# Kernel optimization log

Measured on AMD Instinct MI355X. Metric: run time of the kernel, lower is better.

The kernel has to match this reference:

```python
import jax, jax.numpy as jnp
import numpy as np

DIM = 1024
HEADS = 16
SEQ = 1024
N_EXP = 2
SLOTS = SEQ // N_EXP  # slots per expert; total slots == seq_len as in SoftMoE(dim, seq_len, num_experts)
HID = 4 * DIM         # expert FFN hidden
EPS = 1e-5


def layernorm(x, g, b):
    mu = x.mean(-1, keepdims=True)
    var = x.var(-1, keepdims=True)
    return (x - mu) * jax.lax.rsqrt(var + EPS) * g + b


def setup_inputs() -> dict:
    key = jax.random.key(0)
    ks = jax.random.split(key, 16)
    s = lambda k, shape, scale=0.02: jax.random.normal(k, shape, jnp.float32) * scale
    return {
        "x": jax.random.normal(ks[0], (4, SEQ, DIM), jnp.float32),
        "Wq": s(ks[1], (DIM, DIM)), "bq": jnp.zeros((DIM,), jnp.float32),
        "Wkv": s(ks[2], (DIM, 2 * DIM)), "bkv": jnp.zeros((2 * DIM,), jnp.float32),
        "Wp": s(ks[3], (DIM, DIM)), "bp": jnp.zeros((DIM,), jnp.float32),
        "g1": jnp.ones((DIM,), jnp.float32), "b1": jnp.zeros((DIM,), jnp.float32),
        "phi": s(ks[4], (DIM, N_EXP, SLOTS)),
        "We1": s(ks[5], (N_EXP, DIM, HID)), "be1": jnp.zeros((N_EXP, HID), jnp.float32),
        "We2": s(ks[6], (N_EXP, HID, DIM)), "be2": jnp.zeros((N_EXP, DIM), jnp.float32),
        "g2": jnp.ones((DIM,), jnp.float32), "b2": jnp.zeros((DIM,), jnp.float32),
    }


def soft_moe(x, phi, We1, be1, We2, be2):
    # x: [b,n,d]; phi: [d,e,s]
    logits = jnp.einsum("bnd,des->bnes", x, phi)
    dispatch = jax.nn.softmax(logits, axis=1)                    # over sequence
    b, n, e, s = logits.shape
    combine = jax.nn.softmax(logits.reshape(b, n, e * s), axis=-1).reshape(b, n, e, s)
    slots = jnp.einsum("bnd,bnes->besd", x, dispatch)            # [b,e,s,d]
    h = jax.nn.gelu(jnp.einsum("besd,edh->besh", slots, We1) + be1[None, :, None, :])
    y = jnp.einsum("besh,ehd->besd", h, We2) + be2[None, :, None, :]
    return jnp.einsum("besd,bnes->bnd", y, combine)


def reference(x, Wq, bq, Wkv, bkv, Wp, bp, g1, b1, phi, We1, be1, We2, be2, g2, b2):
    b, n, c = x.shape
    hd = c // HEADS
    scale = hd ** -0.5
    q = (x @ Wq + bq).reshape(b, n, HEADS, hd)
    kv = (x @ Wkv + bkv).reshape(b, n, 2, HEADS, hd)
    k, v = kv[:, :, 0], kv[:, :, 1]
    attn = jnp.einsum("bnhd,bmhd->bnmh", q, k) * scale
    attn = jax.nn.softmax(attn, axis=2)
    out = jnp.einsum("bnmh,bmhd->bnhd", attn, v).reshape(b, n, c)
    out = out @ Wp + bp
    x1 = layernorm(out + x, g1, b1)
    x2 = x1 + soft_moe(x1, phi, We1, be1, We2, be2)
    y = layernorm(x2 + x1, g2, b2)
    return (y, attn)
```

## Files before the change

kernel.cpp:

```cpp
#include <hip/hip_runtime.h>
#include <math.h>

#define BATCH 4
#define SEQ   1024
#define DIM   1024
#define HEADS 16
#define HD    64
#define NEXP  2
#define NSLOT 512
#define ES    1024
#define HID   4096
#define LNEPS 1e-5f
#define NTOK  (BATCH*SEQ)

typedef long long ll;
typedef unsigned short ushort;
typedef unsigned int uint;
typedef __attribute__((ext_vector_type(8))) short short8;
typedef __attribute__((ext_vector_type(4))) float f32x4;
typedef __attribute__((ext_vector_type(4))) unsigned short us4;

__device__ __forceinline__ ushort f2b(float f) {
    uint u = __builtin_bit_cast(uint, f);
    u += 0x7FFFu + ((u >> 16) & 1u);
    return (ushort)(u >> 16);
}
__device__ __forceinline__ float b2f(ushort h) {
    uint u = ((uint)h) << 16;
    return __builtin_bit_cast(float, u);
}
__device__ __forceinline__ uint pk(float a, float b) {
    return (uint)f2b(a) | ((uint)f2b(b) << 16);
}
__device__ __forceinline__ float gelu_f(float v) {
    float x3 = v * v * v;
    return 0.5f * v * (1.f + tanhf(0.7978845608028654f * (v + 0.044715f * x3)));
}

__device__ __forceinline__ void gload16(const ushort* g, ushort* l) {
    __builtin_amdgcn_global_load_lds(
        (const __attribute__((address_space(1))) unsigned int*)(const void*)g,
        (__attribute__((address_space(3))) unsigned int*)(void*)l,
        16, 0, 0);
}

__global__ __launch_bounds__(256) void cvt_bf16(
    const float* __restrict__ src, ushort* __restrict__ dst)
{
    int i = blockIdx.x * 256 + threadIdx.x;
    const float4* s = reinterpret_cast<const float4*>(src) + (ll)i * 2;
    float4 a = s[0], b = s[1];
    uint4 w;
    w.x = pk(a.x, a.y); w.y = pk(a.z, a.w);
    w.z = pk(b.x, b.y); w.w = pk(b.z, b.w);
    reinterpret_cast<uint4*>(dst)[i] = w;
}

__global__ __launch_bounds__(256) void concat_bias(
    const float* __restrict__ a, const float* __restrict__ b,
    float* __restrict__ o)
{
    int i = blockIdx.x * 256 + threadIdx.x;
    o[i] = (i < DIM) ? a[i] : b[i - DIM];
}

template<typename TS, typename TD>
__global__ __launch_bounds__(256) void transpose_cvt(
    const TS* __restrict__ src, int ldsrc, ll sS1, ll sS2,
    TD* __restrict__ dst, int lddst, ll sD1, ll sD2, int Z2)
{
    __shared__ TD tile[64][68];
    const int z1 = blockIdx.z / Z2, z2 = blockIdx.z % Z2;
    src += z1 * sS1 + z2 * sS2;
    dst += z1 * sD1 + z2 * sD2;
    const int r0 = blockIdx.y * 64, c0 = blockIdx.x * 64;
    const int t = threadIdx.x;
    #pragma unroll
    for (int j = 0; j < 4; j++) {
        int idx = t + 256 * j;
        int r = idx >> 4, c = (idx & 15) * 4;
        if constexpr (sizeof(TS) == 4 && sizeof(TD) == 2) {
            float4 v = *reinterpret_cast<const float4*>(src + (ll)(r0 + r) * ldsrc + c0 + c);
            tile[r][c]     = f2b(v.x);
            tile[r][c + 1] = f2b(v.y);
            tile[r][c + 2] = f2b(v.z);
            tile[r][c + 3] = f2b(v.w);
        } else if constexpr (sizeof(TS) == 4 && sizeof(TD) == 4) {
            float4 v = *reinterpret_cast<const float4*>(src + (ll)(r0 + r) * ldsrc + c0 + c);
            *reinterpret_cast<float4*>(&tile[r][c]) = v;
        } else {
            *reinterpret_cast<us4*>(&tile[r][c]) =
                *reinterpret_cast<const us4*>(src + (ll)(r0 + r) * ldsrc + c0 + c);
        }
    }
    __syncthreads();
    #pragma unroll
    for (int j = 0; j < 4; j++) {
        int idx = t + 256 * j;
        int rr = idx >> 4, cc = (idx & 15) * 4;
        if constexpr (sizeof(TD) == 2) {
            us4 w;
            w.x = tile[cc][rr]; w.y = tile[cc + 1][rr];
            w.z = tile[cc + 2][rr]; w.w = tile[cc + 3][rr];
            *reinterpret_cast<us4*>(&dst[(ll)(c0 + rr) * lddst + r0 + cc]) = w;
        } else {
            float4 w;
            w.x = tile[cc][rr]; w.y = tile[cc + 1][rr];
            w.z = tile[cc + 2][rr]; w.w = tile[cc + 3][rr];
            *reinterpret_cast<float4*>(&dst[(ll)(c0 + rr) * lddst + r0 + cc]) = w;
        }
    }
}

template<int WR, int WC, int MI, int NI, int ACT, typename TC>
__global__ __launch_bounds__(256) void gemm_bf16(
    const ushort* __restrict__ A, int lda, ll sA1, ll sA2,
    const ushort* __restrict__ B, int ldb, ll sB1, ll sB2,
    const float* __restrict__ bias, ll sb1, ll sb2,
    TC* __restrict__ C, int ldc, ll sC1, ll sC2,
    int K, int Z2, float alpha)
{
    constexpr int BM = WR * MI * 16;
    constexpr int BN = WC * NI * 16;
    __shared__ alignas(16) ushort As[BM * 32];
    __shared__ alignas(16) ushort Bs[BN * 32];

    const int z1 = blockIdx.z / Z2, z2 = blockIdx.z % Z2;
    A += z1 * sA1 + z2 * sA2;
    B += z1 * sB1 + z2 * sB2;
    C += z1 * sC1 + z2 * sC2;

    const int t = threadIdx.x;
    const int m0 = blockIdx.y * BM, n0 = blockIdx.x * BN;
    const int lane = t & 63, wave = t >> 6;
    const int quad = lane >> 4, l16 = lane & 15;
    const int wm = wave / WC, wn = wave % WC;

    f32x4 acc[MI][NI] = {};

    for (int k0 = 0; k0 < K; k0 += 32) {
        #pragma unroll
        for (int i = 0; i < BM / 64; i++) {
            int seg = i * 256 + t;
            int row = seg >> 2, ke = (seg & 3) * 8;
            gload16(A + (ll)(m0 + row) * lda + (k0 + ke), &As[seg * 8]);
        }
        #pragma unroll
        for (int i = 0; i < BN / 64; i++) {
            int seg = i * 256 + t;
            int row = seg >> 2, ke = (seg & 3) * 8;
            gload16(B + (ll)(n0 + row) * ldb + (k0 + ke), &Bs[seg * 8]);
        }
        __syncthreads();

        short8 a[MI], b[NI];
        #pragma unroll
        for (int mi = 0; mi < MI; mi++)
            a[mi] = *reinterpret_cast<const short8*>(
                &As[(wm * MI * 16 + mi * 16 + l16) * 32 + quad * 8]);
        #pragma unroll
        for (int ni = 0; ni < NI; ni++)
            b[ni] = *reinterpret_cast<const short8*>(
                &Bs[(wn * NI * 16 + ni * 16 + l16) * 32 + quad * 8]);
        #pragma unroll
        for (int mi = 0; mi < MI; mi++)
            #pragma unroll
            for (int ni = 0; ni < NI; ni++)
                acc[mi][ni] = __builtin_amdgcn_mfma_f32_16x16x32_bf16(
                    a[mi], b[ni], acc[mi][ni], 0, 0, 0);
        __syncthreads();
    }

    const float* bz = bias ? (bias + z1 * sb1 + z2 * sb2) : nullptr;
    #pragma unroll
    for (int mi = 0; mi < MI; mi++) {
        #pragma unroll
        for (int ni = 0; ni < NI; ni++) {
            const int row = m0 + wm * MI * 16 + mi * 16 + quad * 4;
            const int col = n0 + wn * NI * 16 + ni * 16 + l16;
            const float bv = bz ? bz[col] : 0.f;
            #pragma unroll
            for (int r = 0; r < 4; r++) {
                float v = alpha * acc[mi][ni][r] + bv;
                if (ACT) v = gelu_f(v);
                if constexpr (sizeof(TC) == 2)
                    C[(ll)(row + r) * ldc + col] = f2b(v);
                else
                    C[(ll)(row + r) * ldc + col] = v;
            }
        }
    }
}

template<int BM, int BN, int ACT, typename TC>
__global__ __launch_bounds__(512) void gemm2(
    const ushort* __restrict__ A, int lda, ll sA1, ll sA2,
    const ushort* __restrict__ B, int ldb, ll sB1, ll sB2,
    const float* __restrict__ bias, ll sb1, ll sb2,
    TC* __restrict__ C, int ldc, ll sC1, ll sC2,
    int K, int Z2, float alpha)
{
    constexpr int WR = BM / 64;
    constexpr int WC = 8 / WR;
    constexpr int MI = 4;
    constexpr int NI = BN / WC / 16;
    constexpr int NH = NI / 2 ? NI / 2 : 1;
    constexpr int LA = BM / 64;
    constexpr int LB = BN / 64;

    __shared__ alignas(16) ushort As[3][BM * 64];
    __shared__ alignas(16) ushort Bs[3][BN * 64];

    const int z1 = blockIdx.z / Z2, z2 = blockIdx.z % Z2;
    A += z1 * sA1 + z2 * sA2;
    B += z1 * sB1 + z2 * sB2;
    C += z1 * sC1 + z2 * sC2;

    const int t = threadIdx.x;
    const int lane = t & 63, wave = t >> 6;
    const int quad = lane >> 4, l16 = lane & 15;
    const int wm = wave / WC, wn = wave % WC;
    const int m0 = blockIdx.y * BM, n0 = blockIdx.x * BN;

    auto stageA = [&](int kt) {
        const ushort* src = A + (ll)m0 * lda + kt * 64;
        ushort* dst = As[kt % 3];
        #pragma unroll
        for (int j = 0; j < LA; j++) {
            int seg = j * 512 + t;
            int row = seg >> 3, kk = (seg & 7) * 8;
            gload16(src + (ll)row * lda + kk, dst + seg * 8);
        }
    };
    auto stageB = [&](int kt) {
        const ushort* src = B + (ll)n0 * ldb + kt * 64;
        ushort* dst = Bs[kt % 3];
        #pragma unroll
        for (int j = 0; j < LB; j++) {
            int seg = j * 512 + t;
            int row = seg >> 3, kk = (seg & 7) * 8;
            gload16(src + (ll)row * ldb + kk, dst + seg * 8);
        }
    };

    f32x4 acc[MI][NI] = {};
    const int NK = K / 64;

    stageA(0); stageB(0);
    if (NK > 1) { stageA(1); stageB(1); }

    for (int kt = 0; kt < NK; kt++) {
        if (kt + 1 < NK)
            asm volatile("s_waitcnt vmcnt(%0)" :: "n"(LA + LB) : "memory");
        else
            asm volatile("s_waitcnt vmcnt(0)" ::: "memory");
        __builtin_amdgcn_sched_barrier(0);
        __builtin_amdgcn_s_barrier();
        __builtin_amdgcn_sched_barrier(0);

        const ushort* Abuf = As[kt % 3];
        const ushort* Bbuf = Bs[kt % 3];

        short8 a[MI][2], b0[NH][2];
        #pragma unroll
        for (int mi = 0; mi < MI; mi++)
            #pragma unroll
            for (int kh = 0; kh < 2; kh++)
                a[mi][kh] = *reinterpret_cast<const short8*>(
                    &Abuf[(wm * 64 + mi * 16 + l16) * 64 + kh * 32 + quad * 8]);
        #pragma unroll
        for (int ni = 0; ni < NH; ni++)
            #pragma unroll
            for (int kh = 0; kh < 2; kh++)
                b0[ni][kh] = *reinterpret_cast<const short8*>(
                    &Bbuf[(wn * NI * 16 + ni * 16 + l16) * 64 + kh * 32 + quad * 8]);
        if (kt + 2 < NK) stageA(kt + 2);
        asm volatile("s_waitcnt lgkmcnt(0)" ::: "memory");
        __builtin_amdgcn_sched_barrier(0);
        __builtin_amdgcn_s_setprio(1);
        #pragma unroll
        for (int mi = 0; mi < MI; mi++)
            #pragma unroll
            for (int ni = 0; ni < NH; ni++)
                #pragma unroll
                for (int kh = 0; kh < 2; kh++)
                    acc[mi][ni] = __builtin_amdgcn_mfma_f32_16x16x32_bf16(
                        a[mi][kh], b0[ni][kh], acc[mi][ni], 0, 0, 0);
        __builtin_amdgcn_s_setprio(0);
        __builtin_amdgcn_sched_barrier(0);

        short8 b1[NH][2];
        #pragma unroll
        for (int ni = 0; ni < NH; ni++)
            #pragma unroll
            for (int kh = 0; kh < 2; kh++)
                b1[ni][kh] = *reinterpret_cast<const short8*>(
                    &Bbuf[(wn * NI * 16 + (NH + ni) * 16 + l16) * 64 + kh * 32 + quad * 8]);
        if (kt + 2 < NK) stageB(kt + 2);
        asm volatile("s_waitcnt lgkmcnt(0)" ::: "memory");
        __builtin_amdgcn_sched_barrier(0);
        __builtin_amdgcn_s_setprio(1);
        #pragma unroll
        for (int mi = 0; mi < MI; mi++)
            #pragma unroll
            for (int ni = 0; ni < NH; ni++)
                #pragma unroll
                for (int kh = 0; kh < 2; kh++)
                    acc[mi][NH + ni] = __builtin_amdgcn_mfma_f32_16x16x32_bf16(
                        a[mi][kh], b1[ni][kh], acc[mi][NH + ni], 0, 0, 0);
        __builtin_amdgcn_s_setprio(0);
        __builtin_amdgcn_sched_barrier(0);
    }

    const float* bz = bias ? (bias + z1 * sb1 + z2 * sb2) : nullptr;
    #pragma unroll
    for (int mi = 0; mi < MI; mi++) {
        #pragma unroll
        for (int ni = 0; ni < NI; ni++) {
            const int row = m0 + wm * 64 + mi * 16 + quad * 4;
            const int col = n0 + wn * NI * 16 + ni * 16 + l16;
            const float bv = bz ? bz[col] : 0.f;
            #pragma unroll
            for (int r = 0; r < 4; r++) {
                float v = alpha * acc[mi][ni][r] + bv;
                if (ACT) v = gelu_f(v);
                if constexpr (sizeof(TC) == 2)
                    C[(ll)(row + r) * ldc + col] = f2b(v);
                else
                    C[(ll)(row + r) * ldc + col] = v;
            }
        }
    }
}

__global__ __launch_bounds__(256) void attn_softmax(
    ushort* __restrict__ p, float* __restrict__ attn_out)
{
    __shared__ float tile[16][1024];
    const int n = blockIdx.x, b = blockIdx.y;
    const int t = threadIdx.x;
    const int lane = t & 63, w = t >> 6;
    ushort* base = p + ((ll)(b * SEQ + n) * HEADS) * SEQ;
    #pragma unroll 1
    for (int g = 0; g < 4; g++) {
        const int h = g * 4 + w;
        ushort* row = base + (ll)h * SEQ + lane * 16;
        uint4 r0 = reinterpret_cast<const uint4*>(row)[0];
        uint4 r1 = reinterpret_cast<const uint4*>(row)[1];
        uint rr[8] = {r0.x, r0.y, r0.z, r0.w, r1.x, r1.y, r1.z, r1.w};
        float v[16];
        float m = -3.0e38f;
        #pragma unroll
        for (int j = 0; j < 8; j++) {
            v[2 * j]     = b2f((ushort)(rr[j] & 0xFFFFu));
            v[2 * j + 1] = b2f((ushort)(rr[j] >> 16));
            m = fmaxf(m, fmaxf(v[2 * j], v[2 * j + 1]));
        }
        #pragma unroll
        for (int o = 32; o; o >>= 1) m = fmaxf(m, __shfl_xor(m, o));
        float s = 0.f;
        #pragma unroll
        for (int j = 0; j < 16; j++) { v[j] = __expf(v[j] - m); s += v[j]; }
        #pragma unroll
        for (int o = 32; o; o >>= 1) s += __shfl_xor(s, o);
        const float inv = 1.f / s;
        #pragma unroll
        for (int j = 0; j < 16; j++) v[j] *= inv;
        uint pw[8];
        #pragma unroll
        for (int j = 0; j < 8; j++) pw[j] = pk(v[2 * j], v[2 * j + 1]);
        uint4 w0, w1;
        w0.x = pw[0]; w0.y = pw[1]; w0.z = pw[2]; w0.w = pw[3];
        w1.x = pw[4]; w1.y = pw[5]; w1.z = pw[6]; w1.w = pw[7];
        reinterpret_cast<uint4*>(row)[0] = w0;
        reinterpret_cast<uint4*>(row)[1] = w1;
        #pragma unroll
        for (int jj = 0; jj < 4; jj++) {
            float4 f4;
            f4.x = v[4 * jj]; f4.y = v[4 * jj + 1];
            f4.z = v[4 * jj + 2]; f4.w = v[4 * jj + 3];
            *reinterpret_cast<float4*>(&tile[h][(jj * 64 + lane) * 4]) = f4;
        }
    }
    __syncthreads();
    float* outp = attn_out + ((ll)b * SEQ + n) * SEQ * HEADS;
    #pragma unroll
    for (int jj = 0; jj < 4; jj++) {
        const int mm = t + 256 * jj;
        const int gm = mm >> 2;
        const int fi = ((gm & 3) * 64 + (gm >> 2)) * 4 + (mm & 3);
        float o16[16];
        #pragma unroll
        for (int h = 0; h < 16; h++) o16[h] = tile[h][fi];
        float4* dst = reinterpret_cast<float4*>(outp + (ll)mm * HEADS);
        #pragma unroll
        for (int q = 0; q < 4; q++) {
            float4 o4;
            o4.x = o16[4 * q]; o4.y = o16[4 * q + 1];
            o4.z = o16[4 * q + 2]; o4.w = o16[4 * q + 3];
            dst[q] = o4;
        }
    }
}

__global__ __launch_bounds__(256) void ln_kernel(
    const float* __restrict__ a, const float* __restrict__ b, float coef,
    const float* __restrict__ g, const float* __restrict__ beta,
    float* __restrict__ out, ushort* __restrict__ out_bf)
{
    const int row = blockIdx.x;
    const int t = threadIdx.x;
    float4 av = reinterpret_cast<const float4*>(a + (ll)row * DIM)[t];
    float4 bv = reinterpret_cast<const float4*>(b + (ll)row * DIM)[t];
    float4 v;
    v.x = av.x + coef * bv.x; v.y = av.y + coef * bv.y;
    v.z = av.z + coef * bv.z; v.w = av.w + coef * bv.w;
    float s1 = v.x + v.y + v.z + v.w;
    float s2 = v.x * v.x + v.y * v.y + v.z * v.z + v.w * v.w;
    __shared__ float red[8];
    #pragma unroll
    for (int o = 32; o; o >>= 1) { s1 += __shfl_xor(s1, o); s2 += __shfl_xor(s2, o); }
    int w = t >> 6;
    if ((t & 63) == 0) { red[w] = s1; red[4 + w] = s2; }
    __syncthreads();
    s1 = red[0] + red[1] + red[2] + red[3];
    s2 = red[4] + red[5] + red[6] + red[7];
    float mu = s1 * (1.f / DIM);
    float var = s2 * (1.f / DIM) - mu * mu;
    float rs = rsqrtf(var + LNEPS);
    float4 gv = reinterpret_cast<const float4*>(g)[t];
    float4 be = reinterpret_cast<const float4*>(beta)[t];
    float4 o;
    o.x = (v.x - mu) * rs * gv.x + be.x;
    o.y = (v.y - mu) * rs * gv.y + be.y;
    o.z = (v.z - mu) * rs * gv.z + be.z;
    o.w = (v.w - mu) * rs * gv.w + be.w;
    reinterpret_cast<float4*>(out + (ll)row * DIM)[t] = o;
    if (out_bf) {
        us4 hv;
        hv.x = f2b(o.x); hv.y = f2b(o.y); hv.z = f2b(o.z); hv.w = f2b(o.w);
        reinterpret_cast<us4*>(out_bf + (ll)row * DIM)[t] = hv;
    }
}

__global__ __launch_bounds__(256) void row_softmax(
    const float* __restrict__ logits, ushort* __restrict__ comb)
{
    const int row = blockIdx.x;
    const int t = threadIdx.x;
    float4 v = reinterpret_cast<const float4*>(logits + (ll)row * 1024)[t];
    float m = fmaxf(fmaxf(v.x, v.y), fmaxf(v.z, v.w));
    __shared__ float red[8];
    #pragma unroll
    for (int o = 32; o; o >>= 1) m = fmaxf(m, __shfl_xor(m, o));
    int w = t >> 6;
    if ((t & 63) == 0) red[w] = m;
    __syncthreads();
    m = fmaxf(fmaxf(red[0], red[1]), fmaxf(red[2], red[3]));
    __syncthreads();
    float4 e;
    e.x = __expf(v.x - m); e.y = __expf(v.y - m);
    e.z = __expf(v.z - m); e.w = __expf(v.w - m);
    float s = e.x + e.y + e.z + e.w;
    #pragma unroll
    for (int o = 32; o; o >>= 1) s += __shfl_xor(s, o);
    if ((t & 63) == 0) red[4 + w] = s;
    __syncthreads();
    s = red[4] + red[5] + red[6] + red[7];
    float inv = 1.f / s;
    us4 hv;
    hv.x = f2b(e.x * inv); hv.y = f2b(e.y * inv);
    hv.z = f2b(e.z * inv); hv.w = f2b(e.w * inv);
    reinterpret_cast<us4*>(comb + (ll)row * 1024)[t] = hv;
}

extern "C" void kernel_launch(void* const* d_in, const int* in_sizes, int n_in,
                              void* d_out, int out_size, void* d_ws, size_t ws_size,
                              hipStream_t stream)
{
    const float* x   = (const float*)d_in[0];
    const float* Wq  = (const float*)d_in[1];
    const float* bq  = (const float*)d_in[2];
    const float* Wkv = (const float*)d_in[3];
    const float* bkv = (const float*)d_in[4];
    const float* Wp  = (const float*)d_in[5];
    const float* bp  = (const float*)d_in[6];
    const float* g1  = (const float*)d_in[7];
    const float* b1  = (const float*)d_in[8];
    const float* phi = (const float*)d_in[9];
    const float* We1 = (const float*)d_in[10];
    const float* be1 = (const float*)d_in[11];
    const float* We2 = (const float*)d_in[12];
    const float* be2 = (const float*)d_in[13];
    const float* g2  = (const float*)d_in[14];
    const float* b2  = (const float*)d_in[15];

    float* out_y    = (float*)d_out;
    float* out_attn = out_y + (ll)BATCH * SEQ * DIM;

    const ll M1 = 1024 * 1024;
    float*  ws     = (float*)d_ws;
    ushort* x_bf   = (ushort*)(ws);
    ushort* WqkvT  = (ushort*)(ws + 2 * M1);
    ushort* WpT    = (ushort*)(ws + 7 * M1 / 2);
    ushort* phiT   = (ushort*)(ws + 4 * M1);
    ushort* qkv_bf = (ushort*)(ws + 9 * M1 / 2);
    ushort* vT     = (ushort*)(ws + 21 * M1 / 2);
    ushort* p_bf   = (ushort*)(ws + 25 * M1 / 2);
    float*  po     = ws + 25 * M1 / 2;
    float*  logitT = ws + 25 * M1 / 2;
    ushort* ao_bf  = (ushort*)(ws + 89 * M1 / 2);
    ushort* ymoeT  = (ushort*)(ws + 89 * M1 / 2);
    float*  x1     = ws + 33 * M1 / 2;
    ushort* x1_bf  = (ushort*)(ws + 41 * M1 / 2);
    ushort* x1T    = (ushort*)(ws + 45 * M1 / 2);
    float*  logit  = ws + 49 * M1 / 2;
    ushort* dispT  = (ushort*)(ws + 57 * M1 / 2);
    ushort* comb   = (ushort*)(ws + 61 * M1 / 2);
    ushort* slots  = (ushort*)(ws + 65 * M1 / 2);
    ushort* hmid   = (ushort*)(ws + 69 * M1 / 2);
    ushort* ymoe   = (ushort*)(ws + 85 * M1 / 2);
    ushort* We1T   = (ushort*)(ws + 9 * M1 / 2);
    ushort* We2T   = (ushort*)(ws + 17 * M1 / 2);
    float*  bqkv   = ws + 93 * M1 / 2;
    float*  moe    = ws;

    dim3 blk(256), blk5(512);

    cvt_bf16<<<dim3(2048), blk, 0, stream>>>(x, x_bf);
    transpose_cvt<float,ushort><<<dim3(16, 16, 1), blk, 0, stream>>>(
        Wq, DIM, 0, 0, WqkvT, DIM, 0, 0, 1);
    transpose_cvt<float,ushort><<<dim3(32, 16, 1), blk, 0, stream>>>(
        Wkv, 2 * DIM, 0, 0, WqkvT + (ll)DIM * DIM, DIM, 0, 0, 1);
    transpose_cvt<float,ushort><<<dim3(16, 16, 1), blk, 0, stream>>>(
        Wp, DIM, 0, 0, WpT, DIM, 0, 0, 1);
    transpose_cvt<float,ushort><<<dim3(16, 16, 1), blk, 0, stream>>>(
        phi, ES, 0, 0, phiT, DIM, 0, 0, 1);
    concat_bias<<<dim3(12), blk, 0, stream>>>(bq, bkv, bqkv);

    gemm2<256,128,0,ushort><<<dim3(24, 16, 1), blk5, 0, stream>>>(
        x_bf, DIM, 0, 0, WqkvT, DIM, 0, 0, bqkv, 0, 0,
        qkv_bf, 3 * DIM, 0, 0, DIM, 1, 1.f);

    transpose_cvt<ushort,ushort><<<dim3(1, 16, BATCH * HEADS), blk, 0, stream>>>(
        qkv_bf + 2 * DIM, 3 * DIM, (ll)SEQ * 3 * DIM, HD,
        vT, SEQ, (ll)HEADS * HD * SEQ, (ll)HD * SEQ, HEADS);

    gemm_bf16<2,2,4,4,0,ushort><<<dim3(8, 8, BATCH * HEADS), blk, 0, stream>>>(
        qkv_bf, 3 * DIM, (ll)SEQ * 3 * DIM, HD,
        qkv_bf + DIM, 3 * DIM, (ll)SEQ * 3 * DIM, HD,
        nullptr, 0, 0,
        p_bf, HEADS * SEQ, (ll)SEQ * HEADS * SEQ, (ll)SEQ,
        HD, HEADS, 0.125f);

    attn_softmax<<<dim3(SEQ, BATCH), blk, 0, stream>>>(p_bf, out_attn);

    gemm2<256,64,0,ushort><<<dim3(1, 4, BATCH * HEADS), blk5, 0, stream>>>(
        p_bf, HEADS * SEQ, (ll)SEQ * HEADS * SEQ, (ll)SEQ,
        vT, SEQ, (ll)HEADS * HD * SEQ, (ll)HD * SEQ,
        nullptr, 0, 0,
        ao_bf, DIM, (ll)SEQ * DIM, HD,
        SEQ, HEADS, 1.f);

    gemm2<128,128,0,float><<<dim3(8, 32, 1), blk5, 0, stream>>>(
        ao_bf, DIM, 0, 0, WpT, DIM, 0, 0, bp, 0, 0,
        po, DIM, 0, 0, DIM, 1, 1.f);
    ln_kernel<<<dim3(NTOK), blk, 0, stream>>>(po, x, 1.0f, g1, b1, x1, x1_bf);

    transpose_cvt<float,ushort><<<dim3(64, 16, 2), blk, 0, stream>>>(
        We1, HID, 0, (ll)DIM * HID, We1T, DIM, 0, (ll)HID * DIM, 2);
    transpose_cvt<float,ushort><<<dim3(16, 64, 2), blk, 0, stream>>>(
        We2, DIM, 0, (ll)HID * DIM, We2T, HID, 0, (ll)DIM * HID, 2);
    transpose_cvt<ushort,ushort><<<dim3(16, 16, BATCH), blk, 0, stream>>>(
        x1_bf, DIM, (ll)SEQ * DIM, 0, x1T, SEQ, (ll)DIM * SEQ, 0, 1);

    gemm2<128,128,0,float><<<dim3(8, 32, 1), blk5, 0, stream>>>(
        x1_bf, DIM, 0, 0, phiT, DIM, 0, 0, nullptr, 0, 0,
        logit, ES, 0, 0, DIM, 1, 1.f);

    transpose_cvt<float,float><<<dim3(16, 16, BATCH), blk, 0, stream>>>(
        logit, ES, (ll)SEQ * ES, 0, logitT, SEQ, (ll)ES * SEQ, 0, 1);
    row_softmax<<<dim3(BATCH * ES), blk, 0, stream>>>(logitT, dispT);
    row_softmax<<<dim3(NTOK), blk, 0, stream>>>(logit, comb);

    gemm2<128,128,0,ushort><<<dim3(8, 8, BATCH), blk5, 0, stream>>>(
        dispT, SEQ, (ll)ES * SEQ, 0,
        x1T, SEQ, (ll)DIM * SEQ, 0,
        nullptr, 0, 0,
        slots, DIM, (ll)ES * DIM, 0,
        SEQ, 1, 1.f);

    gemm2<256,128,1,ushort><<<dim3(32, 2, BATCH * NEXP), blk5, 0, stream>>>(
        slots, DIM, (ll)ES * DIM, (ll)NSLOT * DIM,
        We1T, DIM, 0, (ll)HID * DIM,
        be1, 0, HID,
        hmid, HID, (ll)ES * HID, (ll)NSLOT * HID,
        DIM, NEXP, 1.f);

    gemm2<128,128,0,ushort><<<dim3(8, 4, BATCH * NEXP), blk5, 0, stream>>>(
        hmid, HID, (ll)ES * HID, (ll)NSLOT * HID,
        We2T, HID, 0, (ll)DIM * HID,
        be2, 0, DIM,
        ymoe, DIM, (ll)ES * DIM, (ll)NSLOT * DIM,
        HID, NEXP, 1.f);

    transpose_cvt<ushort,ushort><<<dim3(16, 16, BATCH), blk, 0, stream>>>(
        ymoe, DIM, (ll)ES * DIM, 0, ymoeT, ES, (ll)DIM * ES, 0, 1);

    gemm2<128,128,0,float><<<dim3(8, 8, BATCH), blk5, 0, stream>>>(
        comb, ES, (ll)SEQ * ES, 0,
        ymoeT, ES, (ll)DIM * ES, 0,
        nullptr, 0, 0,
        moe, DIM, (ll)SEQ * DIM, 0,
        ES, 1, 1.f);

    ln_kernel<<<dim3(NTOK), blk, 0, stream>>>(moe, x1, 2.0f, g2, b2, out_y, nullptr);
}
```

Measured before the change: 883.6 us.

## Replace 512-thread triple-buffered GEMMs with 256-thread double-buffered gemm2d kernel

After: 940.7 us. 1.06x slower.

```diff
diff --git a/kernel.cpp b/kernel.cpp
--- a/kernel.cpp
+++ b/kernel.cpp
@@ -112,18 +112,21 @@
     }
 }
 
-template<int WR, int WC, int MI, int NI, int ACT, typename TC>
-__global__ __launch_bounds__(256) void gemm_bf16(
+template<int BM, int BN, int NBUF, int ACT, typename TC>
+__global__ __launch_bounds__(256) void gemm2d(
     const ushort* __restrict__ A, int lda, ll sA1, ll sA2,
     const ushort* __restrict__ B, int ldb, ll sB1, ll sB2,
     const float* __restrict__ bias, ll sb1, ll sb2,
     TC* __restrict__ C, int ldc, ll sC1, ll sC2,
     int K, int Z2, float alpha)
 {
-    constexpr int BM = WR * MI * 16;
-    constexpr int BN = WC * NI * 16;
-    __shared__ alignas(16) ushort As[BM * 32];
-    __shared__ alignas(16) ushort Bs[BN * 32];
+    constexpr int MI = BM / 32;
+    constexpr int NI = BN / 32;
+    constexpr int LA = BM / 32;
+    constexpr int LB = BN / 32;
+
+    __shared__ alignas(16) ushort As[NBUF][BM * 64];
+    __shared__ alignas(16) ushort Bs[NBUF][BN * 64];
 
     const int z1 = blockIdx.z / Z2, z2 = blockIdx.z % Z2;
     A += z1 * sA1 + z2 * sA2;
@@ -131,113 +134,27 @@
     C += z1 * sC1 + z2 * sC2;
 
     const int t = threadIdx.x;
-    const int m0 = blockIdx.y * BM, n0 = blockIdx.x * BN;
     const int lane = t & 63, wave = t >> 6;
     const int quad = lane >> 4, l16 = lane & 15;
-    const int wm = wave / WC, wn = wave % WC;
-
-    f32x4 acc[MI][NI] = {};
-
-    for (int k0 = 0; k0 < K; k0 += 32) {
-        #pragma unroll
-        for (int i = 0; i < BM / 64; i++) {
-            int seg = i * 256 + t;
-            int row = seg >> 2, ke = (seg & 3) * 8;
-            gload16(A + (ll)(m0 + row) * lda + (k0 + ke), &As[seg * 8]);
-        }
-        #pragma unroll
-        for (int i = 0; i < BN / 64; i++) {
-            int seg = i * 256 + t;
-            int row = seg >> 2, ke = (seg & 3) * 8;
-            gload16(B + (ll)(n0 + row) * ldb + (k0 + ke), &Bs[seg * 8]);
-        }
-        __syncthreads();
-
-        short8 a[MI], b[NI];
-        #pragma unroll
-        for (int mi = 0; mi < MI; mi++)
-            a[mi] = *reinterpret_cast<const short8*>(
-                &As[(wm * MI * 16 + mi * 16 + l16) * 32 + quad * 8]);
-        #pragma unroll
-        for (int ni = 0; ni < NI; ni++)
-            b[ni] = *reinterpret_cast<const short8*>(
-                &Bs[(wn * NI * 16 + ni * 16 + l16) * 32 + quad * 8]);
-        #pragma unroll
-        for (int mi = 0; mi < MI; mi++)
-            #pragma unroll
-            for (int ni = 0; ni < NI; ni++)
-                acc[mi][ni] = __builtin_amdgcn_mfma_f32_16x16x32_bf16(
-                    a[mi], b[ni], acc[mi][ni], 0, 0, 0);
-        __syncthreads();
-    }
-
-    const float* bz = bias ? (bias + z1 * sb1 + z2 * sb2) : nullptr;
-    #pragma unroll
-    for (int mi = 0; mi < MI; mi++) {
-        #pragma unroll
-        for (int ni = 0; ni < NI; ni++) {
-            const int row = m0 + wm * MI * 16 + mi * 16 + quad * 4;
-            const int col = n0 + wn * NI * 16 + ni * 16 + l16;
-            const float bv = bz ? bz[col] : 0.f;
-            #pragma unroll
-            for (int r = 0; r < 4; r++) {
-                float v = alpha * acc[mi][ni][r] + bv;
-                if (ACT) v = gelu_f(v);
-                if constexpr (sizeof(TC) == 2)
-                    C[(ll)(row + r) * ldc + col] = f2b(v);
-                else
-                    C[(ll)(row + r) * ldc + col] = v;
-            }
-        }
-    }
-}
-
-template<int BM, int BN, int ACT, typename TC>
-__global__ __launch_bounds__(512) void gemm2(
-    const ushort* __restrict__ A, int lda, ll sA1, ll sA2,
-    const ushort* __restrict__ B, int ldb, ll sB1, ll sB2,
-    const float* __restrict__ bias, ll sb1, ll sb2,
-    TC* __restrict__ C, int ldc, ll sC1, ll sC2,
-    int K, int Z2, float alpha)
-{
-    constexpr int WR = BM / 64;
-    constexpr int WC = 8 / WR;
-    constexpr int MI = 4;
-    constexpr int NI = BN / WC / 16;
-    constexpr int NH = NI / 2 ? NI / 2 : 1;
-    constexpr int LA = BM / 64;
-    constexpr int LB = BN / 64;
-
-    __shared__ alignas(16) ushort As[3][BM * 64];
-    __shared__ alignas(16) ushort Bs[3][BN * 64];
-
-    const int z1 = blockIdx.z / Z2, z2 = blockIdx.z % Z2;
-    A += z1 * sA1 + z2 * sA2;
-    B += z1 * sB1 + z2 * sB2;
-    C += z1 * sC1 + z2 * sC2;
-
-    const int t = threadIdx.x;
-    const int lane = t & 63, wave = t >> 6;
-    const int quad = lane >> 4, l16 = lane & 15;
-    const int wm = wave / WC, wn = wave % WC;
+    const int wm = wave >> 1, wn = wave & 1;
     const int m0 = blockIdx.y * BM, n0 = blockIdx.x * BN;
 
     auto stageA = [&](int kt) {
         const ushort* src = A + (ll)m0 * lda + kt * 64;
-        ushort* dst = As[kt % 3];
+        ushort* dst = As[kt & (NBUF - 1)];
         #pragma unroll
         for (int j = 0; j < LA; j++) {
-            int seg = j * 512 + t;
+            int seg = j * 256 + t;
             int row = seg >> 3, kk = (seg & 7) * 8;
             gload16(src + (ll)row * lda + kk, dst + seg * 8);
         }
     };
     auto stageB = [&](int kt) {
         const ushort* src = B + (ll)n0 * ldb + kt * 64;
-        ushort* dst = Bs[kt % 3];
+        ushort* dst = Bs[kt & (NBUF - 1)];
         #pragma unroll
         for (int j = 0; j < LB; j++) {
-            int seg = j * 512 + t;
+            int seg = j * 256 + t;
             int row = seg >> 3, kk = (seg & 7) * 8;
             gload16(src + (ll)row * ldb + kk, dst + seg * 8);
         }
@@ -247,21 +164,17 @@
     const int NK = K / 64;
 
     stageA(0); stageB(0);
-    if (NK > 1) { stageA(1); stageB(1); }
+    asm volatile("s_waitcnt vmcnt(0)" ::: "memory");
+    __builtin_amdgcn_sched_barrier(0);
+    __builtin_amdgcn_s_barrier();
+    __builtin_amdgcn_sched_barrier(0);
 
     for (int kt = 0; kt < NK; kt++) {
-        if (kt + 1 < NK)
-            asm volatile("s_waitcnt vmcnt(%0)" :: "n"(LA + LB) : "memory");
-        else
-            asm volatile("s_waitcnt vmcnt(0)" ::: "memory");
-        __builtin_amdgcn_sched_barrier(0);
-        __builtin_amdgcn_s_barrier();
-        __builtin_amdgcn_sched_barrier(0);
-
-        const ushort* Abuf = As[kt % 3];
-        const ushort* Bbuf = Bs[kt % 3];
-
-        short8 a[MI][2], b0[NH][2];
+        if (kt + 1 < NK) { stageA(kt + 1); stageB(kt + 1); }
+
+        const ushort* Abuf = As[kt & (NBUF - 1)];
+        const ushort* Bbuf = Bs[kt & (NBUF - 1)];
+        short8 a[MI][2], b[NI][2];
         #pragma unroll
         for (int mi = 0; mi < MI; mi++)
             #pragma unroll
@@ -269,47 +182,31 @@
                 a[mi][kh] = *reinterpret_cast<const short8*>(
                     &Abuf[(wm * 64 + mi * 16 + l16) * 64 + kh * 32 + quad * 8]);
         #pragma unroll
-        for (int ni = 0; ni < NH; ni++)
+        for (int ni = 0; ni < NI; ni++)
             #pragma unroll
             for (int kh = 0; kh < 2; kh++)
-                b0[ni][kh] = *reinterpret_cast<const short8*>(
+                b[ni][kh] = *reinterpret_cast<const short8*>(
                     &Bbuf[(wn * NI * 16 + ni * 16 + l16) * 64 + kh * 32 + quad * 8]);
-        if (kt + 2 < NK) stageA(kt + 2);
         asm volatile("s_waitcnt lgkmcnt(0)" ::: "memory");
         __builtin_amdgcn_sched_barrier(0);
         __builtin_amdgcn_s_setprio(1);
         #pragma unroll
         for (int mi = 0; mi < MI; mi++)
             #pragma unroll
-            for (int ni = 0; ni < NH; ni++)
+            for (int ni = 0; ni < NI; ni++)
                 #pragma unroll
                 for (int kh = 0; kh < 2; kh++)
                     acc[mi][ni] = __builtin_amdgcn_mfma_f32_16x16x32_bf16(
-                        a[mi][kh], b0[ni][kh], acc[mi][ni], 0, 0, 0);
+                        a[mi][kh], b[ni][kh], acc[mi][ni], 0, 0, 0);
         __builtin_amdgcn_s_setprio(0);
         __builtin_amdgcn_sched_barrier(0);
 
-        short8 b1[NH][2];
-        #pragma unroll
-        for (int ni = 0; ni < NH; ni++)
-            #pragma unroll
-            for (int kh = 0; kh < 2; kh++)
-                b1[ni][kh] = *reinterpret_cast<const short8*>(
-                    &Bbuf[(wn * NI * 16 + (NH + ni) * 16 + l16) * 64 + kh * 32 + quad * 8]);
-        if (kt + 2 < NK) stageB(kt + 2);
-        asm volatile("s_waitcnt lgkmcnt(0)" ::: "memory");
-        __builtin_amdgcn_sched_barrier(0);
-        __builtin_amdgcn_s_setprio(1);
-        #pragma unroll
-        for (int mi = 0; mi < MI; mi++)
-            #pragma unroll
-            for (int ni = 0; ni < NH; ni++)
-                #pragma unroll
-                for (int kh = 0; kh < 2; kh++)
-                    acc[mi][NH + ni] = __builtin_amdgcn_mfma_f32_16x16x32_bf16(
-                        a[mi][kh], b1[ni][kh], acc[mi][NH + ni], 0, 0, 0);
-        __builtin_amdgcn_s_setprio(0);
-        __builtin_amdgcn_sched_barrier(0);
+        if (kt + 1 < NK) {
+            asm volatile("s_waitcnt vmcnt(0)" ::: "memory");
+            __builtin_amdgcn_sched_barrier(0);
+            __builtin_amdgcn_s_barrier();
+            __builtin_amdgcn_sched_barrier(0);
+        }
     }
 
     const float* bz = bias ? (bias + z1 * sb1 + z2 * sb2) : nullptr;
@@ -525,7 +422,7 @@
     float*  bqkv   = ws + 93 * M1 / 2;
     float*  moe    = ws;
 
-    dim3 blk(256), blk5(512);
+    dim3 blk(256);
 
     cvt_bf16<<<dim3(2048), blk, 0, stream>>>(x, x_bf);
     transpose_cvt<float,ushort><<<dim3(16, 16, 1), blk, 0, stream>>>(
@@ -538,7 +435,7 @@
         phi, ES, 0, 0, phiT, DIM, 0, 0, 1);
     concat_bias<<<dim3(12), blk, 0, stream>>>(bq, bkv, bqkv);
 
-    gemm2<256,128,0,ushort><<<dim3(24, 16, 1), blk5, 0, stream>>>(
+    gemm2d<128,128,2,0,ushort><<<dim3(24, 32, 1), blk, 0, stream>>>(
         x_bf, DIM, 0, 0, WqkvT, DIM, 0, 0, bqkv, 0, 0,
         qkv_bf, 3 * DIM, 0, 0, DIM, 1, 1.f);
 
@@ -546,7 +443,7 @@
         qkv_bf + 2 * DIM, 3 * DIM, (ll)SEQ * 3 * DIM, HD,
         vT, SEQ, (ll)HEADS * HD * SEQ, (ll)HD * SEQ, HEADS);
 
-    gemm_bf16<2,2,4,4,0,ushort><<<dim3(8, 8, BATCH * HEADS), blk, 0, stream>>>(
+    gemm2d<128,128,1,0,ushort><<<dim3(8, 8, BATCH * HEADS), blk, 0, stream>>>(
         qkv_bf, 3 * DIM, (ll)SEQ * 3 * DIM, HD,
         qkv_bf + DIM, 3 * DIM, (ll)SEQ * 3 * DIM, HD,
         nullptr, 0, 0,
@@ -555,14 +452,14 @@
 
     attn_softmax<<<dim3(SEQ, BATCH), blk, 0, stream>>>(p_bf, out_attn);
 
-    gemm2<256,64,0,ushort><<<dim3(1, 4, BATCH * HEADS), blk5, 0, stream>>>(
+    gemm2d<128,64,2,0,ushort><<<dim3(1, 8, BATCH * HEADS), blk, 0, stream>>>(
         p_bf, HEADS * SEQ, (ll)SEQ * HEADS * SEQ, (ll)SEQ,
         vT, SEQ, (ll)HEADS * HD * SEQ, (ll)HD * SEQ,
         nullptr, 0, 0,
         ao_bf, DIM, (ll)SEQ * DIM, HD,
         SEQ, HEADS, 1.f);
 
-    gemm2<128,128,0,float><<<dim3(8, 32, 1), blk5, 0, stream>>>(
+    gemm2d<128,128,2,0,float><<<dim3(8, 32, 1), blk, 0, stream>>>(
         ao_bf, DIM, 0, 0, WpT, DIM, 0, 0, bp, 0, 0,
         po, DIM, 0, 0, DIM, 1, 1.f);
     ln_kernel<<<dim3(NTOK), blk, 0, stream>>>(po, x, 1.0f, g1, b1, x1, x1_bf);
@@ -574,7 +471,7 @@
     transpose_cvt<ushort,ushort><<<dim3(16, 16, BATCH), blk, 0, stream>>>(
         x1_bf, DIM, (ll)SEQ * DIM, 0, x1T, SEQ, (ll)DIM * SEQ, 0, 1);
 
-    gemm2<128,128,0,float><<<dim3(8, 32, 1), blk5, 0, stream>>>(
+    gemm2d<128,128,2,0,float><<<dim3(8, 32, 1), blk, 0, stream>>>(
         x1_bf, DIM, 0, 0, phiT, DIM, 0, 0, nullptr, 0, 0,
         logit, ES, 0, 0, DIM, 1, 1.f);
 
@@ -583,21 +480,21 @@
     row_softmax<<<dim3(BATCH * ES), blk, 0, stream>>>(logitT, dispT);
     row_softmax<<<dim3(NTOK), blk, 0, stream>>>(logit, comb);
 
-    gemm2<128,128,0,ushort><<<dim3(8, 8, BATCH), blk5, 0, stream>>>(
+    gemm2d<128,128,2,0,ushort><<<dim3(8, 8, BATCH), blk, 0, stream>>>(
         dispT, SEQ, (ll)ES * SEQ, 0,
         x1T, SEQ, (ll)DIM * SEQ, 0,
         nullptr, 0, 0,
         slots, DIM, (ll)ES * DIM, 0,
         SEQ, 1, 1.f);
 
-    gemm2<256,128,1,ushort><<<dim3(32, 2, BATCH * NEXP), blk5, 0, stream>>>(
+    gemm2d<128,128,2,1,ushort><<<dim3(32, 4, BATCH * NEXP), blk, 0, stream>>>(
         slots, DIM, (ll)ES * DIM, (ll)NSLOT * DIM,
         We1T, DIM, 0, (ll)HID * DIM,
         be1, 0, HID,
         hmid, HID, (ll)ES * HID, (ll)NSLOT * HID,
         DIM, NEXP, 1.f);
 
-    gemm2<128,128,0,ushort><<<dim3(8, 4, BATCH * NEXP), blk5, 0, stream>>>(
+    gemm2d<128,128,2,0,ushort><<<dim3(8, 4, BATCH * NEXP), blk, 0, stream>>>(
         hmid, HID, (ll)ES * HID, (ll)NSLOT * HID,
         We2T, HID, 0, (ll)DIM * HID,
         be2, 0, DIM,
@@ -607,7 +504,7 @@
     transpose_cvt<ushort,ushort><<<dim3(16, 16, BATCH), blk, 0, stream>>>(
         ymoe, DIM, (ll)ES * DIM, 0, ymoeT, ES, (ll)DIM * ES, 0, 1);
 
-    gemm2<128,128,0,float><<<dim3(8, 8, BATCH), blk5, 0, stream>>>(
+    gemm2d<128,128,2,0,float><<<dim3(8, 8, BATCH), blk, 0, stream>>>(
         comb, ES, (ll)SEQ * ES, 0,
         ymoeT, ES, (ll)DIM * ES, 0,
         nullptr, 0, 0,
```
